# Optimization experiments

Hardware: AMD Instinct MI355X
Metric: run time of the kernel (lower is better)

## Reference

```python
import jax, jax.numpy as jnp
import numpy as np

H = 2048          # hidden_size
N = 16384         # batch (= events processed in one forward)
THR = 0.7         # event_threshold
NEG = -1e30       # masked-softmax fill


def setup_inputs() -> dict:
    key = jax.random.key(0)
    ks = jax.random.split(key, 8)
    s = lambda k, shape, scale: (jax.random.normal(k, shape, dtype=jnp.float32) * scale)
    return {
        "x": jax.random.normal(ks[0], (N, H), dtype=jnp.float32),
        "importance": jax.random.uniform(ks[1], (N,), dtype=jnp.float32),
        # event_detector: Linear(H, H//2) -> ReLU -> Linear(H//2, 1) -> Sigmoid
        "W_e1": s(ks[2], (H, H // 2), 0.02), "b_e1": jnp.zeros((H // 2,), jnp.float32),
        "W_e2": s(ks[3], (H // 2, 1), 0.05), "b_e2": jnp.ones((1,), jnp.float32),
        # retrieval_network: Linear(H, H//2) -> ReLU -> Linear(H//2, H) -> Sigmoid
        "W_r1": s(ks[4], (H, H // 2), 0.02), "b_r1": jnp.zeros((H // 2,), jnp.float32),
        "W_r2": s(ks[5], (H // 2, H), 0.02), "b_r2": jnp.zeros((H,), jnp.float32),
        "timestamp": 0,
    }


def reference(x, importance, W_e1, b_e1, W_e2, b_e2, W_r1, b_r1, W_r2, b_r2, timestamp):
    # --- detect_events: MLP -> sigmoid -> threshold -------------------------
    scores = jax.nn.sigmoid(jnp.maximum(x @ W_e1 + b_e1, 0.0) @ W_e2 + b_e2)[:, 0]  # [N]
    events = scores > THR                                   # bool mask = event-gated scatter
    has_events = jnp.any(events)

    # --- store_memory + consolidate_memories --------------------------------
    # Event rows are written into the ring buffer (no wraparound since N <= capacity);
    # consolidation = softmax over stored importances, weighted sum of stored rows.
    logits = jnp.where(events, importance, NEG)             # masked softmax over event rows
    w = jax.nn.softmax(logits)                              # [N]
    w = jnp.where(events, w, 0.0)
    consolidated = w @ x                                    # [H]

    # --- retrieve_memory -----------------------------------------------------
    # After consolidation memory_count == 1, so softmax(similarities) == 1 for
    # every query row and retrieved_memory == consolidated (broadcast to [N,H]).
    retrieved = jax.nn.sigmoid(jnp.maximum(consolidated @ W_r1 + b_r1, 0.0) @ W_r2 + b_r2)  # [H]

    # If no events fired, memory_count == 0 and retrieve_memory returns zeros.
    add = jnp.where(has_events, retrieved, jnp.zeros_like(retrieved))
    return x + add[None, :]
```

## Files before the change

### kernel.cpp

```cpp
#include <hip/hip_runtime.h>
#include <hip/hip_bf16.h>

#define H_    2048
#define NROWS 16384
#define HH    1024

typedef __bf16 bf16x8 __attribute__((ext_vector_type(8)));
typedef float  floatx4 __attribute__((ext_vector_type(4)));

__device__ __forceinline__ unsigned f2bf(float f) {
  unsigned u = __builtin_bit_cast(unsigned, f);
  u += 0x7fff + ((u >> 16) & 1);
  return u >> 16;
}

__device__ __forceinline__ void gload_lds16(const void* g, void* l) {
  __builtin_amdgcn_global_load_lds(
      (const __attribute__((address_space(1))) unsigned*)g,
      (__attribute__((address_space(3))) unsigned*)l, 16, 0, 0);
}

__global__ __launch_bounds__(256) void convert_x_kernel(
    const float* __restrict__ x, unsigned short* __restrict__ xb)
{
  size_t base = ((size_t)blockIdx.x * 256 + threadIdx.x) * 8;
#pragma unroll
  for (int it = 0; it < 8; ++it) {
    size_t i = base + (size_t)it * (524288u * 8);
    float4 v0 = *reinterpret_cast<const float4*>(x + i);
    float4 v1 = *reinterpret_cast<const float4*>(x + i + 4);
    uint4 o;
    o.x = f2bf(v0.x) | (f2bf(v0.y) << 16);
    o.y = f2bf(v0.z) | (f2bf(v0.w) << 16);
    o.z = f2bf(v1.x) | (f2bf(v1.y) << 16);
    o.w = f2bf(v1.z) | (f2bf(v1.w) << 16);
    *reinterpret_cast<uint4*>(xb + i) = o;
  }
}

__global__ __launch_bounds__(256) void transpose_w1_kernel(
    const float* __restrict__ W1, unsigned short* __restrict__ W1t)
{
  __shared__ unsigned short tile[64][66];
  int k0 = blockIdx.x * 64;
  int n0 = blockIdx.y * 64;
  int t = threadIdx.x;
#pragma unroll
  for (int i = 0; i < 4; i++) {
    int idx = t + i * 256;
    int r = idx >> 4, c4 = (idx & 15) << 2;
    float4 v = *reinterpret_cast<const float4*>(W1 + (size_t)(k0 + r) * HH + n0 + c4);
    tile[r][c4 + 0] = (unsigned short)f2bf(v.x);
    tile[r][c4 + 1] = (unsigned short)f2bf(v.y);
    tile[r][c4 + 2] = (unsigned short)f2bf(v.z);
    tile[r][c4 + 3] = (unsigned short)f2bf(v.w);
  }
  __syncthreads();
#pragma unroll
  for (int i = 0; i < 2; i++) {
    int idx = t + i * 256;
    int n = idx >> 3, k8 = (idx & 7) << 3;
    uint4 o;
    o.x = (unsigned)tile[k8 + 0][n] | ((unsigned)tile[k8 + 1][n] << 16);
    o.y = (unsigned)tile[k8 + 2][n] | ((unsigned)tile[k8 + 3][n] << 16);
    o.z = (unsigned)tile[k8 + 4][n] | ((unsigned)tile[k8 + 5][n] << 16);
    o.w = (unsigned)tile[k8 + 6][n] | ((unsigned)tile[k8 + 7][n] << 16);
    *reinterpret_cast<uint4*>(W1t + (size_t)(n0 + n) * H_ + k0 + k8) = o;
  }
}

__global__ __launch_bounds__(256) void gemm_v2_kernel(
    const unsigned short* __restrict__ xb, const unsigned short* __restrict__ W1t,
    const float* __restrict__ b1, const float* __restrict__ W2,
    float* __restrict__ s_pre)
{
  __shared__ unsigned short As[128 * 64];
  __shared__ unsigned short Bs[128 * 64];

  const int t    = threadIdx.x;
  const int m0   = blockIdx.x * 128;
  const int n0   = blockIdx.y * 128;
  const int wave = t >> 6, lane = t & 63;
  const int wr   = (wave >> 1) * 64;
  const int wc   = (wave & 1) * 64;
  const int lcol = lane & 15, quad = lane >> 4;

  floatx4 acc[4][4] = {};

  const int srow = t >> 3;
  const int sq   = (t & 7) ^ (srow & 7);
  const unsigned short* ag = xb  + (size_t)(m0 + srow) * H_ + sq * 8;
  const unsigned short* bg = W1t + (size_t)(n0 + srow) * H_ + sq * 8;
  unsigned short* al = As + 512 * wave;
  unsigned short* bl = Bs + 512 * wave;

  for (int kk = 0; kk < H_; kk += 64) {
    __syncthreads();
#pragma unroll
    for (int j = 0; j < 4; j++) {
      gload_lds16(ag + kk + (size_t)(32 * j) * H_, al + 2048 * j);
      gload_lds16(bg + kk + (size_t)(32 * j) * H_, bl + 2048 * j);
    }
    __syncthreads();

#pragma unroll
    for (int h = 0; h < 2; h++) {
      bf16x8 af[4], bfr[4];
#pragma unroll
      for (int mt = 0; mt < 4; mt++) {
        int r = wr + mt * 16 + lcol;
        af[mt] = *reinterpret_cast<const bf16x8*>(
            As + r * 64 + ((((h << 2) | quad) ^ (r & 7)) << 3));
      }
#pragma unroll
      for (int nt = 0; nt < 4; nt++) {
        int r = wc + nt * 16 + lcol;
        bfr[nt] = *reinterpret_cast<const bf16x8*>(
            Bs + r * 64 + ((((h << 2) | quad) ^ (r & 7)) << 3));
      }
#pragma unroll
      for (int mt = 0; mt < 4; mt++)
#pragma unroll
        for (int nt = 0; nt < 4; nt++)
          acc[mt][nt] = __builtin_amdgcn_mfma_f32_16x16x32_bf16(af[mt], bfr[nt], acc[mt][nt], 0, 0, 0);
    }
  }

  float rowsum[4][4];
#pragma unroll
  for (int mt = 0; mt < 4; mt++)
#pragma unroll
    for (int r = 0; r < 4; r++) rowsum[mt][r] = 0.f;

#pragma unroll
  for (int nt = 0; nt < 4; nt++) {
    int n = n0 + wc + nt * 16 + lcol;
    float b1v = b1[n], w2v = W2[n];
#pragma unroll
    for (int mt = 0; mt < 4; mt++)
#pragma unroll
      for (int r = 0; r < 4; r++) {
        float h = fmaxf(acc[mt][nt][r] + b1v, 0.f);
        rowsum[mt][r] = fmaf(h, w2v, rowsum[mt][r]);
      }
  }
#pragma unroll
  for (int mt = 0; mt < 4; mt++)
#pragma unroll
    for (int r = 0; r < 4; r++) {
      float s = rowsum[mt][r];
      s += __shfl_xor(s, 1); s += __shfl_xor(s, 2);
      s += __shfl_xor(s, 4); s += __shfl_xor(s, 8);
      if (lcol == 0)
        atomicAdd(&s_pre[m0 + wr + mt * 16 + quad * 4 + r], s);
    }
}

__global__ __launch_bounds__(256) void gemm_score_kernel(
    const float* __restrict__ x, const float* __restrict__ W1,
    const float* __restrict__ b1, const float* __restrict__ W2,
    float* __restrict__ s_pre)
{
  __shared__ unsigned short As[128][40];
  __shared__ unsigned short Bs[128][40];
  const int t    = threadIdx.x;
  const int n0   = blockIdx.x * 128;
  const int m0   = blockIdx.y * 128;
  const int wave = t >> 6, lane = t & 63;
  const int wr   = (wave >> 1) * 64;
  const int wc   = (wave & 1) * 64;
  const int lcol = lane & 15, quad = lane >> 4;
  floatx4 acc[4][4] = {};

  for (int kk = 0; kk < H_; kk += 32) {
    __syncthreads();
#pragma unroll
    for (int i = 0; i < 4; i++) {
      int idx = t + i * 256;
      int row = idx >> 3, k4 = (idx & 7) << 2;
      float4 v = *reinterpret_cast<const float4*>(x + (size_t)(m0 + row) * H_ + kk + k4);
      unsigned lo = f2bf(v.x) | (f2bf(v.y) << 16);
      unsigned hi = f2bf(v.z) | (f2bf(v.w) << 16);
      *reinterpret_cast<uint2*>(&As[row][k4]) = make_uint2(lo, hi);
    }
#pragma unroll
    for (int i = 0; i < 4; i++) {
      int idx = t + i * 256;
      int kr = idx >> 5, c4 = (idx & 31) << 2;
      float4 v = *reinterpret_cast<const float4*>(W1 + (size_t)(kk + kr) * HH + n0 + c4);
      Bs[c4 + 0][kr] = (unsigned short)f2bf(v.x);
      Bs[c4 + 1][kr] = (unsigned short)f2bf(v.y);
      Bs[c4 + 2][kr] = (unsigned short)f2bf(v.z);
      Bs[c4 + 3][kr] = (unsigned short)f2bf(v.w);
    }
    __syncthreads();
    bf16x8 af[4], bfr[4];
#pragma unroll
    for (int mt = 0; mt < 4; mt++)
      af[mt] = *reinterpret_cast<const bf16x8*>(&As[wr + mt * 16 + lcol][quad * 8]);
#pragma unroll
    for (int nt = 0; nt < 4; nt++)
      bfr[nt] = *reinterpret_cast<const bf16x8*>(&Bs[wc + nt * 16 + lcol][quad * 8]);
#pragma unroll
    for (int mt = 0; mt < 4; mt++)
#pragma unroll
      for (int nt = 0; nt < 4; nt++)
        acc[mt][nt] = __builtin_amdgcn_mfma_f32_16x16x32_bf16(af[mt], bfr[nt], acc[mt][nt], 0, 0, 0);
  }
  float rowsum[4][4];
#pragma unroll
  for (int mt = 0; mt < 4; mt++)
#pragma unroll
    for (int r = 0; r < 4; r++) rowsum[mt][r] = 0.f;
#pragma unroll
  for (int nt = 0; nt < 4; nt++) {
    int n = n0 + wc + nt * 16 + lcol;
    float b1v = b1[n], w2v = W2[n];
#pragma unroll
    for (int mt = 0; mt < 4; mt++)
#pragma unroll
      for (int r = 0; r < 4; r++) {
        float h = fmaxf(acc[mt][nt][r] + b1v, 0.f);
        rowsum[mt][r] = fmaf(h, w2v, rowsum[mt][r]);
      }
  }
#pragma unroll
  for (int mt = 0; mt < 4; mt++)
#pragma unroll
    for (int r = 0; r < 4; r++) {
      float s = rowsum[mt][r];
      s += __shfl_xor(s, 1); s += __shfl_xor(s, 2);
      s += __shfl_xor(s, 4); s += __shfl_xor(s, 8);
      if (lcol == 0)
        atomicAdd(&s_pre[m0 + wr + mt * 16 + quad * 4 + r], s);
    }
}

__global__ __launch_bounds__(256) void consolidate_partial_kernel(
    const float* __restrict__ x, const float* __restrict__ s_pre,
    const float* __restrict__ imp, const float* __restrict__ b2,
    float* __restrict__ part, float* __restrict__ Z, float* __restrict__ cnt)
{
  __shared__ float wl[64];
  int t  = threadIdx.x;
  int r0 = blockIdx.x * 64;
  if (t < 64) {
    float s   = s_pre[r0 + t] + b2[0];
    float sig = 1.f / (1.f + __expf(-s));
    bool  ev  = sig > 0.7f;
    float w   = ev ? __expf(imp[r0 + t]) : 0.f;
    wl[t] = w;
    float cw = ev ? 1.f : 0.f;
#pragma unroll
    for (int off = 32; off; off >>= 1) {
      w  += __shfl_down(w, off);
      cw += __shfl_down(cw, off);
    }
    if (t == 0) { atomicAdd(Z, w); atomicAdd(cnt, cw); }
  }
  __syncthreads();

  float a[8] = {0.f, 0.f, 0.f, 0.f, 0.f, 0.f, 0.f, 0.f};
  for (int r = 0; r < 64; ++r) {
    float w = wl[r];
    if (w != 0.f) {
      const float4* xr = reinterpret_cast<const float4*>(x + (size_t)(r0 + r) * H_);
      float4 v0 = xr[t], v1 = xr[t + 256];
      a[0] = fmaf(w, v0.x, a[0]); a[1] = fmaf(w, v0.y, a[1]);
      a[2] = fmaf(w, v0.z, a[2]); a[3] = fmaf(w, v0.w, a[3]);
      a[4] = fmaf(w, v1.x, a[4]); a[5] = fmaf(w, v1.y, a[5]);
      a[6] = fmaf(w, v1.z, a[6]); a[7] = fmaf(w, v1.w, a[7]);
    }
  }
  size_t base = (size_t)blockIdx.x * 2048;
  int j0 = t * 4;
  part[base + j0 + 0] = a[0]; part[base + j0 + 1] = a[1];
  part[base + j0 + 2] = a[2]; part[base + j0 + 3] = a[3];
  part[base + 1024 + j0 + 0] = a[4]; part[base + 1024 + j0 + 1] = a[5];
  part[base + 1024 + j0 + 2] = a[6]; part[base + 1024 + j0 + 3] = a[7];
}

__global__ __launch_bounds__(256) void reduce_c_kernel(
    const float* __restrict__ part, float* __restrict__ c)
{
  int j = blockIdx.x * 256 + threadIdx.x;
  float s = 0.f;
#pragma unroll 8
  for (int b = 0; b < 256; ++b)
    s += part[(size_t)b * 2048 + j];
  c[j] = s;
}

__global__ __launch_bounds__(256) void score_kernel(
    const float* __restrict__ s_pre, const float* __restrict__ imp,
    const float* __restrict__ b2, float* __restrict__ wbuf,
    float* __restrict__ Z, float* __restrict__ cnt)
{
  int i = blockIdx.x * 256 + threadIdx.x;
  float s = s_pre[i] + b2[0];
  float sig = 1.f / (1.f + __expf(-s));
  bool ev = sig > 0.7f;
  float w = ev ? __expf(imp[i]) : 0.f;
  wbuf[i] = w;
  float cw = ev ? 1.f : 0.f;
#pragma unroll
  for (int off = 32; off; off >>= 1) {
    w  += __shfl_down(w, off);
    cw += __shfl_down(cw, off);
  }
  if ((threadIdx.x & 63) == 0) {
    atomicAdd(Z, w);
    atomicAdd(cnt, cw);
  }
}

__global__ __launch_bounds__(256) void consolidate_kernel(
    const float* __restrict__ x, const float* __restrict__ wbuf,
    float* __restrict__ c)
{
  int t = threadIdx.x;
  int r0 = blockIdx.x * 128;
  float a[8] = {0.f, 0.f, 0.f, 0.f, 0.f, 0.f, 0.f, 0.f};
  for (int r = 0; r < 128; r++) {
    float w = wbuf[r0 + r];
    if (w != 0.f) {
      const float4* xr = reinterpret_cast<const float4*>(x + (size_t)(r0 + r) * H_);
      float4 v0 = xr[t], v1 = xr[t + 256];
      a[0] = fmaf(w, v0.x, a[0]); a[1] = fmaf(w, v0.y, a[1]);
      a[2] = fmaf(w, v0.z, a[2]); a[3] = fmaf(w, v0.w, a[3]);
      a[4] = fmaf(w, v1.x, a[4]); a[5] = fmaf(w, v1.y, a[5]);
      a[6] = fmaf(w, v1.z, a[6]); a[7] = fmaf(w, v1.w, a[7]);
    }
  }
  int j0 = t * 4;
  atomicAdd(&c[j0 + 0], a[0]); atomicAdd(&c[j0 + 1], a[1]);
  atomicAdd(&c[j0 + 2], a[2]); atomicAdd(&c[j0 + 3], a[3]);
  atomicAdd(&c[1024 + j0 + 0], a[4]); atomicAdd(&c[1024 + j0 + 1], a[5]);
  atomicAdd(&c[1024 + j0 + 2], a[6]); atomicAdd(&c[1024 + j0 + 3], a[7]);
}

__global__ __launch_bounds__(256) void r1_kernel(
    const float* __restrict__ c, const float* __restrict__ Z,
    const float* __restrict__ cnt, const float* __restrict__ Wr1,
    float* __restrict__ hr)
{
  __shared__ float cs[128];
  int n  = blockIdx.x * 256 + threadIdx.x;
  int k0 = blockIdx.y * 128;
  float inv = (cnt[0] > 0.5f) ? (1.f / Z[0]) : 0.f;
  if (threadIdx.x < 128) cs[threadIdx.x] = c[k0 + threadIdx.x] * inv;
  __syncthreads();
  float s = 0.f;
#pragma unroll 8
  for (int k = 0; k < 128; k++)
    s = fmaf(cs[k], Wr1[(size_t)(k0 + k) * HH + n], s);
  atomicAdd(&hr[n], s);
}

__global__ __launch_bounds__(256) void r2_kernel(
    const float* __restrict__ hr, const float* __restrict__ br1,
    const float* __restrict__ Wr2, float* __restrict__ rt)
{
  __shared__ float hs[128];
  int n  = blockIdx.x * 256 + threadIdx.x;
  int k0 = blockIdx.y * 128;
  if (threadIdx.x < 128)
    hs[threadIdx.x] = fmaxf(hr[k0 + threadIdx.x] + br1[k0 + threadIdx.x], 0.f);
  __syncthreads();
  float s = 0.f;
#pragma unroll 8
  for (int k = 0; k < 128; k++)
    s = fmaf(hs[k], Wr2[(size_t)(k0 + k) * H_ + n], s);
  atomicAdd(&rt[n], s);
}

__global__ __launch_bounds__(256) void finalize_kernel(
    const float* __restrict__ rt, const float* __restrict__ br2,
    const float* __restrict__ cnt, float* __restrict__ addv)
{
  int j = blockIdx.x * 256 + threadIdx.x;
  float v = 0.f;
  if (cnt[0] > 0.5f) v = 1.f / (1.f + expf(-(rt[j] + br2[j])));
  addv[j] = v;
}

__global__ __launch_bounds__(256) void out_kernel(
    const float* __restrict__ x, const float* __restrict__ addv,
    float* __restrict__ out)
{
  size_t base = (size_t)blockIdx.x * 256 + threadIdx.x;
  float4 a = reinterpret_cast<const float4*>(addv)[(int)(base & 511)];
#pragma unroll
  for (int it = 0; it < 16; ++it) {
    size_t i = base + (size_t)it * 524288u;
    float4 v = reinterpret_cast<const float4*>(x)[i];
    v.x += a.x; v.y += a.y; v.z += a.z; v.w += a.w;
    reinterpret_cast<float4*>(out)[i] = v;
  }
}

extern "C" void kernel_launch(void* const* d_in, const int* in_sizes, int n_in,
                              void* d_out, int out_size, void* d_ws, size_t ws_size,
                              hipStream_t stream)
{
  (void)in_sizes; (void)n_in; (void)out_size;
  const float* x   = (const float*)d_in[0];
  const float* imp = (const float*)d_in[1];
  const float* We1 = (const float*)d_in[2];
  const float* be1 = (const float*)d_in[3];
  const float* We2 = (const float*)d_in[4];
  const float* be2 = (const float*)d_in[5];
  const float* Wr1 = (const float*)d_in[6];
  const float* br1 = (const float*)d_in[7];
  const float* Wr2 = (const float*)d_in[8];
  const float* br2 = (const float*)d_in[9];
  float* out = (float*)d_out;

  float* ws    = (float*)d_ws;
  float* s_pre = ws;
  float* c     = ws + 16384;
  float* hr    = ws + 18432;
  float* rt    = ws + 19456;
  float* Z     = ws + 21504;
  float* cnt   = ws + 21505;
  float* wbuf  = ws + 21760;
  float* addv  = ws + 38144;

  const size_t scal_bytes = 49152 * sizeof(float);
  const size_t xb_bytes   = (size_t)NROWS * H_ * 2;
  const size_t w1t_bytes  = (size_t)HH * H_ * 2;
  unsigned short* xb  = (unsigned short*)((char*)d_ws + scal_bytes);
  unsigned short* W1t = (unsigned short*)((char*)d_ws + scal_bytes + xb_bytes);
  float* part = (float*)xb;
  const bool fast = ws_size >= scal_bytes + xb_bytes + w1t_bytes;

  hipMemsetAsync(d_ws, 0, 21506 * sizeof(float), stream);

  if (fast) {
    convert_x_kernel<<<2048, 256, 0, stream>>>(x, xb);
    transpose_w1_kernel<<<dim3(32, 16), 256, 0, stream>>>(We1, W1t);
    gemm_v2_kernel<<<dim3(128, 8), 256, 0, stream>>>(xb, W1t, be1, We2, s_pre);
    consolidate_partial_kernel<<<256, 256, 0, stream>>>(x, s_pre, imp, be2, part, Z, cnt);
    reduce_c_kernel<<<8, 256, 0, stream>>>(part, c);
  } else {
    gemm_score_kernel<<<dim3(8, 128), 256, 0, stream>>>(x, We1, be1, We2, s_pre);
    score_kernel<<<64, 256, 0, stream>>>(s_pre, imp, be2, wbuf, Z, cnt);
    consolidate_kernel<<<128, 256, 0, stream>>>(x, wbuf, c);
  }
  r1_kernel<<<dim3(4, 16), 256, 0, stream>>>(c, Z, cnt, Wr1, hr);
  r2_kernel<<<dim3(8, 8), 256, 0, stream>>>(hr, br1, Wr2, rt);
  finalize_kernel<<<8, 256, 0, stream>>>(rt, br2, cnt, addv);
  out_kernel<<<2048, 256, 0, stream>>>(x, addv, out);
}
```

Before: 443.4 us.

## Replace score GEMM with 256x256 double-buffered ping-pong MFMA kernel, consolidate from bf16

Rewrites the event-score GEMM as a 512-thread kernel on 256x256 tiles. LDS is double-buffered, and global-to-LDS staging is interleaved with MFMA phases using explicit barriers, waitcnt and priority control, so memory latency overlaps compute and more data is reused per tile. The consolidation pass now reads the bf16 copy of x instead of fp32, which halves its traffic but rounds the weighted sum to bf16 precision. The partial-sum buffer moves into the W1t region so it no longer aliases xb.

```diff
diff --git a/kernel.cpp b/kernel.cpp
--- a/kernel.cpp
+++ b/kernel.cpp
@@ -7,11 +7,16 @@
 
 typedef __bf16 bf16x8 __attribute__((ext_vector_type(8)));
 typedef float  floatx4 __attribute__((ext_vector_type(4)));
+typedef unsigned short ushortx8 __attribute__((ext_vector_type(8)));
 
 __device__ __forceinline__ unsigned f2bf(float f) {
   unsigned u = __builtin_bit_cast(unsigned, f);
   u += 0x7fff + ((u >> 16) & 1);
   return u >> 16;
+}
+
+__device__ __forceinline__ float bf2f(unsigned short u) {
+  return __builtin_bit_cast(float, (unsigned)u << 16);
 }
 
 __device__ __forceinline__ void gload_lds16(const void* g, void* l) {
@@ -69,90 +74,142 @@
   }
 }
 
-__global__ __launch_bounds__(256) void gemm_v2_kernel(
+__global__ __launch_bounds__(512, 2) void gemm_v3_kernel(
     const unsigned short* __restrict__ xb, const unsigned short* __restrict__ W1t,
     const float* __restrict__ b1, const float* __restrict__ W2,
     float* __restrict__ s_pre)
 {
-  __shared__ unsigned short As[128 * 64];
-  __shared__ unsigned short Bs[128 * 64];
+  __shared__ unsigned short LA[2][2][8192];
+  __shared__ unsigned short LB[2][2][8192];
 
   const int t    = threadIdx.x;
-  const int m0   = blockIdx.x * 128;
-  const int n0   = blockIdx.y * 128;
-  const int wave = t >> 6, lane = t & 63;
-  const int wr   = (wave >> 1) * 64;
-  const int wc   = (wave & 1) * 64;
+  const int m0   = blockIdx.x * 256;
+  const int n0   = blockIdx.y * 256;
+  const int w    = t >> 6, lane = t & 63;
+  const int wm   = w >> 2;
+  const int wn   = w & 3;
+  const int bh   = wn >> 1;
+  const int bc0  = (wn & 1) * 64;
   const int lcol = lane & 15, quad = lane >> 4;
-
-  floatx4 acc[4][4] = {};
-
-  const int srow = t >> 3;
-  const int sq   = (t & 7) ^ (srow & 7);
-  const unsigned short* ag = xb  + (size_t)(m0 + srow) * H_ + sq * 8;
-  const unsigned short* bg = W1t + (size_t)(n0 + srow) * H_ + sq * 8;
-  unsigned short* al = As + 512 * wave;
-  unsigned short* bl = Bs + 512 * wave;
-
-  for (int kk = 0; kk < H_; kk += 64) {
-    __syncthreads();
-#pragma unroll
-    for (int j = 0; j < 4; j++) {
-      gload_lds16(ag + kk + (size_t)(32 * j) * H_, al + 2048 * j);
-      gload_lds16(bg + kk + (size_t)(32 * j) * H_, bl + 2048 * j);
-    }
-    __syncthreads();
-
-#pragma unroll
-    for (int h = 0; h < 2; h++) {
-      bf16x8 af[4], bfr[4];
-#pragma unroll
-      for (int mt = 0; mt < 4; mt++) {
-        int r = wr + mt * 16 + lcol;
-        af[mt] = *reinterpret_cast<const bf16x8*>(
-            As + r * 64 + ((((h << 2) | quad) ^ (r & 7)) << 3));
-      }
-#pragma unroll
-      for (int nt = 0; nt < 4; nt++) {
-        int r = wc + nt * 16 + lcol;
-        bfr[nt] = *reinterpret_cast<const bf16x8*>(
-            Bs + r * 64 + ((((h << 2) | quad) ^ (r & 7)) << 3));
-      }
-#pragma unroll
-      for (int mt = 0; mt < 4; mt++)
-#pragma unroll
-        for (int nt = 0; nt < 4; nt++)
-          acc[mt][nt] = __builtin_amdgcn_mfma_f32_16x16x32_bf16(af[mt], bfr[nt], acc[mt][nt], 0, 0, 0);
-    }
-  }
-
-  float rowsum[4][4];
-#pragma unroll
-  for (int mt = 0; mt < 4; mt++)
-#pragma unroll
-    for (int r = 0; r < 4; r++) rowsum[mt][r] = 0.f;
-
-#pragma unroll
-  for (int nt = 0; nt < 4; nt++) {
-    int n = n0 + wc + nt * 16 + lcol;
+  const int sx   = lane & 7;
+
+  const int rloc = w * 8 + (lane >> 3);
+  const int qoff = ((lane & 7) ^ (rloc & 7)) * 8;
+  const unsigned short* aS = xb  + (size_t)(m0 + rloc) * H_ + qoff;
+  const unsigned short* bS = W1t + (size_t)(n0 + rloc) * H_ + qoff;
+  const int wj0 = w * 512, wj1 = 4096 + w * 512;
+
+  floatx4 acc[8][4] = {};
+  bf16x8 af[4][2];
+  bf16x8 bq[2][2][2];
+
+#define STG_A(P, h, T) do { \
+    gload_lds16(aS + (size_t)((h) * 128) * H_ + (T) * 64,        &LA[P][h][wj0]); \
+    gload_lds16(aS + (size_t)((h) * 128 + 64) * H_ + (T) * 64,   &LA[P][h][wj1]); } while (0)
+#define STG_B(P, h, T) do { \
+    gload_lds16(bS + (size_t)((h) * 128) * H_ + (T) * 64,        &LB[P][h][wj0]); \
+    gload_lds16(bS + (size_t)((h) * 128 + 64) * H_ + (T) * 64,   &LB[P][h][wj1]); } while (0)
+
+#define RD_A4(P, base) do { _Pragma("unroll") \
+    for (int mi = 0; mi < 4; ++mi) { \
+      const int rr = ((base) + mi) * 16 + lcol; \
+      af[mi][0] = *reinterpret_cast<const bf16x8*>(&LA[P][wm][rr * 64 + ((quad) ^ sx) * 8]); \
+      af[mi][1] = *reinterpret_cast<const bf16x8*>(&LA[P][wm][rr * 64 + ((4 + quad) ^ sx) * 8]); } } while (0)
+#define RD_B2(P, g) do { _Pragma("unroll") \
+    for (int ni = 0; ni < 2; ++ni) { \
+      const int cc = bc0 + ((g) * 2 + ni) * 16 + lcol; \
+      bq[g][ni][0] = *reinterpret_cast<const bf16x8*>(&LB[P][bh][cc * 64 + ((quad) ^ sx) * 8]); \
+      bq[g][ni][1] = *reinterpret_cast<const bf16x8*>(&LB[P][bh][cc * 64 + ((4 + quad) ^ sx) * 8]); } } while (0)
+
+#define MFMA_Q(mg, ng) do { _Pragma("unroll") \
+    for (int mi = 0; mi < 4; ++mi) { _Pragma("unroll") \
+      for (int ni = 0; ni < 2; ++ni) { \
+        acc[(mg)*4+mi][(ng)*2+ni] = __builtin_amdgcn_mfma_f32_16x16x32_bf16(af[mi][0], bq[ng][ni][0], acc[(mg)*4+mi][(ng)*2+ni], 0, 0, 0); \
+        acc[(mg)*4+mi][(ng)*2+ni] = __builtin_amdgcn_mfma_f32_16x16x32_bf16(af[mi][1], bq[ng][ni][1], acc[(mg)*4+mi][(ng)*2+ni], 0, 0, 0); } } } while (0)
+
+#define PH_PRE() do { asm volatile("" ::: "memory"); __builtin_amdgcn_s_barrier(); \
+    asm volatile("s_waitcnt lgkmcnt(0)" ::: "memory"); \
+    __builtin_amdgcn_sched_barrier(0); __builtin_amdgcn_s_setprio(1); } while (0)
+#define PH_POST() do { __builtin_amdgcn_s_setprio(0); \
+    asm volatile("" ::: "memory"); __builtin_amdgcn_s_barrier(); } while (0)
+
+#define CKPT(ST) do { \
+    __builtin_amdgcn_s_setprio(0); \
+    if (ST) asm volatile("s_waitcnt vmcnt(6)" ::: "memory"); \
+    else    asm volatile("s_waitcnt vmcnt(0)" ::: "memory"); \
+    asm volatile("" ::: "memory"); __builtin_amdgcn_s_barrier(); } while (0)
+
+#define BODY(Ta, Tb, ST) do { \
+     \
+    RD_A4(0, 0); RD_B2(0, 0); \
+    STG_A(1, 1, Tb); \
+    PH_PRE(); MFMA_Q(0, 0); PH_POST(); \
+     \
+    RD_B2(0, 1); \
+    PH_PRE(); MFMA_Q(0, 1); PH_POST(); \
+     \
+    RD_A4(0, 4); \
+    if (ST) STG_B(0, 0, (Ta) + 2); \
+    PH_PRE(); MFMA_Q(1, 1); PH_POST(); \
+     \
+    if (ST) { STG_B(0, 1, (Ta) + 2); STG_A(0, 0, (Ta) + 2); } \
+    PH_PRE(); MFMA_Q(1, 0); CKPT(ST); \
+     \
+    RD_A4(1, 0); RD_B2(1, 0); \
+    if (ST) STG_A(0, 1, (Ta) + 2); \
+    PH_PRE(); MFMA_Q(0, 0); PH_POST(); \
+     \
+    RD_B2(1, 1); \
+    PH_PRE(); MFMA_Q(0, 1); PH_POST(); \
+     \
+    RD_A4(1, 4); \
+    if (ST) STG_B(1, 0, (Tb) + 2); \
+    PH_PRE(); MFMA_Q(1, 1); PH_POST(); \
+     \
+    if (ST) { STG_B(1, 1, (Tb) + 2); STG_A(1, 0, (Tb) + 2); } \
+    PH_PRE(); MFMA_Q(1, 0); CKPT(ST); } while (0)
+
+  STG_A(0, 0, 0); STG_A(0, 1, 0); STG_B(0, 0, 0); STG_B(0, 1, 0);
+  STG_B(1, 0, 1); STG_B(1, 1, 1); STG_A(1, 0, 1);
+  asm volatile("s_waitcnt vmcnt(6)" ::: "memory");
+  __builtin_amdgcn_s_barrier();
+
+#pragma unroll 1
+  for (int i = 0; i < 15; ++i) {
+    BODY(2 * i, 2 * i + 1, 1);
+  }
+  BODY(30, 31, 0);
+
+#undef STG_A
+#undef STG_B
+#undef RD_A4
+#undef RD_B2
+#undef MFMA_Q
+#undef PH_PRE
+#undef PH_POST
+#undef CKPT
+#undef BODY
+
+  float rs[8][4] = {};
+#pragma unroll
+  for (int nf = 0; nf < 4; ++nf) {
+    int n = n0 + wn * 64 + nf * 16 + lcol;
     float b1v = b1[n], w2v = W2[n];
 #pragma unroll
-    for (int mt = 0; mt < 4; mt++)
-#pragma unroll
-      for (int r = 0; r < 4; r++) {
-        float h = fmaxf(acc[mt][nt][r] + b1v, 0.f);
-        rowsum[mt][r] = fmaf(h, w2v, rowsum[mt][r]);
-      }
-  }
-#pragma unroll
-  for (int mt = 0; mt < 4; mt++)
-#pragma unroll
-    for (int r = 0; r < 4; r++) {
-      float s = rowsum[mt][r];
+    for (int mf = 0; mf < 8; ++mf)
+#pragma unroll
+      for (int r = 0; r < 4; ++r)
+        rs[mf][r] = fmaf(fmaxf(acc[mf][nf][r] + b1v, 0.f), w2v, rs[mf][r]);
+  }
+#pragma unroll
+  for (int mf = 0; mf < 8; ++mf)
+#pragma unroll
+    for (int r = 0; r < 4; ++r) {
+      float s = rs[mf][r];
       s += __shfl_xor(s, 1); s += __shfl_xor(s, 2);
       s += __shfl_xor(s, 4); s += __shfl_xor(s, 8);
       if (lcol == 0)
-        atomicAdd(&s_pre[m0 + wr + mt * 16 + quad * 4 + r], s);
+        atomicAdd(&s_pre[m0 + wm * 128 + mf * 16 + quad * 4 + r], s);
     }
 }
 
@@ -237,7 +294,7 @@
 }
 
 __global__ __launch_bounds__(256) void consolidate_partial_kernel(
-    const float* __restrict__ x, const float* __restrict__ s_pre,
+    const unsigned short* __restrict__ xb, const float* __restrict__ s_pre,
     const float* __restrict__ imp, const float* __restrict__ b2,
     float* __restrict__ part, float* __restrict__ Z, float* __restrict__ cnt)
 {
@@ -264,20 +321,15 @@
   for (int r = 0; r < 64; ++r) {
     float w = wl[r];
     if (w != 0.f) {
-      const float4* xr = reinterpret_cast<const float4*>(x + (size_t)(r0 + r) * H_);
-      float4 v0 = xr[t], v1 = xr[t + 256];
-      a[0] = fmaf(w, v0.x, a[0]); a[1] = fmaf(w, v0.y, a[1]);
-      a[2] = fmaf(w, v0.z, a[2]); a[3] = fmaf(w, v0.w, a[3]);
-      a[4] = fmaf(w, v1.x, a[4]); a[5] = fmaf(w, v1.y, a[5]);
-      a[6] = fmaf(w, v1.z, a[6]); a[7] = fmaf(w, v1.w, a[7]);
-    }
-  }
-  size_t base = (size_t)blockIdx.x * 2048;
-  int j0 = t * 4;
-  part[base + j0 + 0] = a[0]; part[base + j0 + 1] = a[1];
-  part[base + j0 + 2] = a[2]; part[base + j0 + 3] = a[3];
-  part[base + 1024 + j0 + 0] = a[4]; part[base + 1024 + j0 + 1] = a[5];
-  part[base + 1024 + j0 + 2] = a[6]; part[base + 1024 + j0 + 3] = a[7];
+      ushortx8 v = *reinterpret_cast<const ushortx8*>(
+          xb + (size_t)(r0 + r) * H_ + t * 8);
+#pragma unroll
+      for (int e = 0; e < 8; ++e) a[e] = fmaf(w, bf2f(v[e]), a[e]);
+    }
+  }
+  size_t base = (size_t)blockIdx.x * 2048 + t * 8;
+#pragma unroll
+  for (int e = 0; e < 8; ++e) part[base + e] = a[e];
 }
 
 __global__ __launch_bounds__(256) void reduce_c_kernel(
@@ -431,7 +483,7 @@
   const size_t w1t_bytes  = (size_t)HH * H_ * 2;
   unsigned short* xb  = (unsigned short*)((char*)d_ws + scal_bytes);
   unsigned short* W1t = (unsigned short*)((char*)d_ws + scal_bytes + xb_bytes);
-  float* part = (float*)xb;
+  float* part = (float*)W1t;
   const bool fast = ws_size >= scal_bytes + xb_bytes + w1t_bytes;
 
   hipMemsetAsync(d_ws, 0, 21506 * sizeof(float), stream);
@@ -439,8 +491,8 @@
   if (fast) {
     convert_x_kernel<<<2048, 256, 0, stream>>>(x, xb);
     transpose_w1_kernel<<<dim3(32, 16), 256, 0, stream>>>(We1, W1t);
-    gemm_v2_kernel<<<dim3(128, 8), 256, 0, stream>>>(xb, W1t, be1, We2, s_pre);
-    consolidate_partial_kernel<<<256, 256, 0, stream>>>(x, s_pre, imp, be2, part, Z, cnt);
+    gemm_v3_kernel<<<dim3(64, 4), 512, 0, stream>>>(xb, W1t, be1, We2, s_pre);
+    consolidate_partial_kernel<<<256, 256, 0, stream>>>(xb, s_pre, imp, be2, part, Z, cnt);
     reduce_c_kernel<<<8, 256, 0, stream>>>(part, c);
   } else {
     gemm_score_kernel<<<dim3(8, 128), 256, 0, stream>>>(x, We1, be1, We2, s_pre);
```

New measurement: 437.0 us. No clear change (-1.4%).

## Enlarge GEMM block to 256x128 with 8 waves and read bf16 x in consolidation

Applied to the files above, without the earlier changes.

The score GEMM now uses 512-thread blocks covering 256 rows by 128 columns. That halves the number of times each W1 tile is reloaded, and the B fragments are held in registers and reused across the M sub-tiles, with s_setprio raised around the MFMA bursts. The consolidation pass now reads the bf16 copy of x instead of fp32, which halves its memory traffic but weights the event rows with bf16-rounded values. The partial-sum buffer is moved onto the W1t region so it no longer overwrites xb, which is still being read.

```diff
diff --git a/kernel.cpp b/kernel.cpp
--- a/kernel.cpp
+++ b/kernel.cpp
@@ -7,11 +7,16 @@
 
 typedef __bf16 bf16x8 __attribute__((ext_vector_type(8)));
 typedef float  floatx4 __attribute__((ext_vector_type(4)));
+typedef unsigned short ushortx8 __attribute__((ext_vector_type(8)));
 
 __device__ __forceinline__ unsigned f2bf(float f) {
   unsigned u = __builtin_bit_cast(unsigned, f);
   u += 0x7fff + ((u >> 16) & 1);
   return u >> 16;
+}
+
+__device__ __forceinline__ float bf2f(unsigned short u) {
+  return __builtin_bit_cast(float, (unsigned)u << 16);
 }
 
 __device__ __forceinline__ void gload_lds16(const void* g, void* l) {
@@ -69,90 +74,87 @@
   }
 }
 
-__global__ __launch_bounds__(256) void gemm_v2_kernel(
+__global__ __launch_bounds__(512, 4) void gemm_v4_kernel(
     const unsigned short* __restrict__ xb, const unsigned short* __restrict__ W1t,
     const float* __restrict__ b1, const float* __restrict__ W2,
     float* __restrict__ s_pre)
 {
-  __shared__ unsigned short As[128 * 64];
+  __shared__ unsigned short As[256 * 64];
   __shared__ unsigned short Bs[128 * 64];
 
   const int t    = threadIdx.x;
-  const int m0   = blockIdx.x * 128;
+  const int m0   = blockIdx.x * 256;
   const int n0   = blockIdx.y * 128;
-  const int wave = t >> 6, lane = t & 63;
-  const int wr   = (wave >> 1) * 64;
-  const int wc   = (wave & 1) * 64;
+  const int w    = t >> 6, lane = t & 63;
+  const int wm   = w >> 1;
+  const int wn   = w & 1;
   const int lcol = lane & 15, quad = lane >> 4;
 
+  const int srow = t >> 3;
+  const int sq   = ((t & 7) ^ (srow & 7)) * 8;
+  const unsigned short* aSb = xb  + (size_t)(m0 + srow) * H_ + sq;
+  const unsigned short* bSb = W1t + (size_t)(n0 + srow) * H_ + sq;
+  unsigned short* al = As + w * 512;
+  unsigned short* bl = Bs + w * 512;
+
   floatx4 acc[4][4] = {};
-
-  const int srow = t >> 3;
-  const int sq   = (t & 7) ^ (srow & 7);
-  const unsigned short* ag = xb  + (size_t)(m0 + srow) * H_ + sq * 8;
-  const unsigned short* bg = W1t + (size_t)(n0 + srow) * H_ + sq * 8;
-  unsigned short* al = As + 512 * wave;
-  unsigned short* bl = Bs + 512 * wave;
 
   for (int kk = 0; kk < H_; kk += 64) {
     __syncthreads();
 #pragma unroll
-    for (int j = 0; j < 4; j++) {
-      gload_lds16(ag + kk + (size_t)(32 * j) * H_, al + 2048 * j);
-      gload_lds16(bg + kk + (size_t)(32 * j) * H_, bl + 2048 * j);
-    }
+    for (int j = 0; j < 4; ++j)
+      gload_lds16(aSb + kk + (size_t)(64 * j) * H_, al + 4096 * j);
+#pragma unroll
+    for (int j = 0; j < 2; ++j)
+      gload_lds16(bSb + kk + (size_t)(64 * j) * H_, bl + 4096 * j);
     __syncthreads();
 
-#pragma unroll
-    for (int h = 0; h < 2; h++) {
-      bf16x8 af[4], bfr[4];
-#pragma unroll
-      for (int mt = 0; mt < 4; mt++) {
-        int r = wr + mt * 16 + lcol;
-        af[mt] = *reinterpret_cast<const bf16x8*>(
-            As + r * 64 + ((((h << 2) | quad) ^ (r & 7)) << 3));
+    bf16x8 bq[4][2];
+#pragma unroll
+    for (int ni = 0; ni < 4; ++ni) {
+      int r = wn * 64 + ni * 16 + lcol;
+#pragma unroll
+      for (int kh = 0; kh < 2; ++kh)
+        bq[ni][kh] = *reinterpret_cast<const bf16x8*>(
+            Bs + r * 64 + (((kh * 4 + quad) ^ (r & 7)) * 8));
+    }
+#pragma unroll
+    for (int mi = 0; mi < 4; ++mi) {
+      int r = wm * 64 + mi * 16 + lcol;
+      bf16x8 a0 = *reinterpret_cast<const bf16x8*>(
+          As + r * 64 + (((quad) ^ (r & 7)) * 8));
+      bf16x8 a1 = *reinterpret_cast<const bf16x8*>(
+          As + r * 64 + (((4 + quad) ^ (r & 7)) * 8));
+      __builtin_amdgcn_s_setprio(1);
+#pragma unroll
+      for (int ni = 0; ni < 4; ++ni) {
+        acc[mi][ni] = __builtin_amdgcn_mfma_f32_16x16x32_bf16(a0, bq[ni][0], acc[mi][ni], 0, 0, 0);
+        acc[mi][ni] = __builtin_amdgcn_mfma_f32_16x16x32_bf16(a1, bq[ni][1], acc[mi][ni], 0, 0, 0);
       }
-#pragma unroll
-      for (int nt = 0; nt < 4; nt++) {
-        int r = wc + nt * 16 + lcol;
-        bfr[nt] = *reinterpret_cast<const bf16x8*>(
-            Bs + r * 64 + ((((h << 2) | quad) ^ (r & 7)) << 3));
-      }
-#pragma unroll
-      for (int mt = 0; mt < 4; mt++)
-#pragma unroll
-        for (int nt = 0; nt < 4; nt++)
-          acc[mt][nt] = __builtin_amdgcn_mfma_f32_16x16x32_bf16(af[mt], bfr[nt], acc[mt][nt], 0, 0, 0);
-    }
-  }
-
-  float rowsum[4][4];
-#pragma unroll
-  for (int mt = 0; mt < 4; mt++)
-#pragma unroll
-    for (int r = 0; r < 4; r++) rowsum[mt][r] = 0.f;
-
-#pragma unroll
-  for (int nt = 0; nt < 4; nt++) {
-    int n = n0 + wc + nt * 16 + lcol;
+      __builtin_amdgcn_s_setprio(0);
+    }
+  }
+
+  float rs[4][4] = {};
+#pragma unroll
+  for (int ni = 0; ni < 4; ++ni) {
+    int n = n0 + wn * 64 + ni * 16 + lcol;
     float b1v = b1[n], w2v = W2[n];
 #pragma unroll
-    for (int mt = 0; mt < 4; mt++)
-#pragma unroll
-      for (int r = 0; r < 4; r++) {
-        float h = fmaxf(acc[mt][nt][r] + b1v, 0.f);
-        rowsum[mt][r] = fmaf(h, w2v, rowsum[mt][r]);
-      }
-  }
-#pragma unroll
-  for (int mt = 0; mt < 4; mt++)
-#pragma unroll
-    for (int r = 0; r < 4; r++) {
-      float s = rowsum[mt][r];
+    for (int mi = 0; mi < 4; ++mi)
+#pragma unroll
+      for (int r = 0; r < 4; ++r)
+        rs[mi][r] = fmaf(fmaxf(acc[mi][ni][r] + b1v, 0.f), w2v, rs[mi][r]);
+  }
+#pragma unroll
+  for (int mi = 0; mi < 4; ++mi)
+#pragma unroll
+    for (int r = 0; r < 4; ++r) {
+      float s = rs[mi][r];
       s += __shfl_xor(s, 1); s += __shfl_xor(s, 2);
       s += __shfl_xor(s, 4); s += __shfl_xor(s, 8);
       if (lcol == 0)
-        atomicAdd(&s_pre[m0 + wr + mt * 16 + quad * 4 + r], s);
+        atomicAdd(&s_pre[m0 + wm * 64 + mi * 16 + quad * 4 + r], s);
     }
 }
 
@@ -237,7 +239,7 @@
 }
 
 __global__ __launch_bounds__(256) void consolidate_partial_kernel(
-    const float* __restrict__ x, const float* __restrict__ s_pre,
+    const unsigned short* __restrict__ xb, const float* __restrict__ s_pre,
     const float* __restrict__ imp, const float* __restrict__ b2,
     float* __restrict__ part, float* __restrict__ Z, float* __restrict__ cnt)
 {
@@ -264,20 +266,15 @@
   for (int r = 0; r < 64; ++r) {
     float w = wl[r];
     if (w != 0.f) {
-      const float4* xr = reinterpret_cast<const float4*>(x + (size_t)(r0 + r) * H_);
-      float4 v0 = xr[t], v1 = xr[t + 256];
-      a[0] = fmaf(w, v0.x, a[0]); a[1] = fmaf(w, v0.y, a[1]);
-      a[2] = fmaf(w, v0.z, a[2]); a[3] = fmaf(w, v0.w, a[3]);
-      a[4] = fmaf(w, v1.x, a[4]); a[5] = fmaf(w, v1.y, a[5]);
-      a[6] = fmaf(w, v1.z, a[6]); a[7] = fmaf(w, v1.w, a[7]);
-    }
-  }
-  size_t base = (size_t)blockIdx.x * 2048;
-  int j0 = t * 4;
-  part[base + j0 + 0] = a[0]; part[base + j0 + 1] = a[1];
-  part[base + j0 + 2] = a[2]; part[base + j0 + 3] = a[3];
-  part[base + 1024 + j0 + 0] = a[4]; part[base + 1024 + j0 + 1] = a[5];
-  part[base + 1024 + j0 + 2] = a[6]; part[base + 1024 + j0 + 3] = a[7];
+      ushortx8 v = *reinterpret_cast<const ushortx8*>(
+          xb + (size_t)(r0 + r) * H_ + t * 8);
+#pragma unroll
+      for (int e = 0; e < 8; ++e) a[e] = fmaf(w, bf2f(v[e]), a[e]);
+    }
+  }
+  size_t base = (size_t)blockIdx.x * 2048 + t * 8;
+#pragma unroll
+  for (int e = 0; e < 8; ++e) part[base + e] = a[e];
 }
 
 __global__ __launch_bounds__(256) void reduce_c_kernel(
@@ -431,7 +428,7 @@
   const size_t w1t_bytes  = (size_t)HH * H_ * 2;
   unsigned short* xb  = (unsigned short*)((char*)d_ws + scal_bytes);
   unsigned short* W1t = (unsigned short*)((char*)d_ws + scal_bytes + xb_bytes);
-  float* part = (float*)xb;
+  float* part = (float*)W1t;
   const bool fast = ws_size >= scal_bytes + xb_bytes + w1t_bytes;
 
   hipMemsetAsync(d_ws, 0, 21506 * sizeof(float), stream);
@@ -439,8 +436,8 @@
   if (fast) {
     convert_x_kernel<<<2048, 256, 0, stream>>>(x, xb);
     transpose_w1_kernel<<<dim3(32, 16), 256, 0, stream>>>(We1, W1t);
-    gemm_v2_kernel<<<dim3(128, 8), 256, 0, stream>>>(xb, W1t, be1, We2, s_pre);
-    consolidate_partial_kernel<<<256, 256, 0, stream>>>(x, s_pre, imp, be2, part, Z, cnt);
+    gemm_v4_kernel<<<dim3(64, 8), 512, 0, stream>>>(xb, W1t, be1, We2, s_pre);
+    consolidate_partial_kernel<<<256, 256, 0, stream>>>(xb, s_pre, imp, be2, part, Z, cnt);
     reduce_c_kernel<<<8, 256, 0, stream>>>(part, c);
   } else {
     gemm_score_kernel<<<dim3(8, 128), 256, 0, stream>>>(x, We1, be1, We2, s_pre);
```

New measurement: 425.9 us. -3.9%, faster.
